# Performance work log

Hardware: AMD Instinct MI355X
Metric: run time of the kernel (lower is better)

Reference implementation:

```python
import jax, jax.numpy as jnp
import numpy as np

B = 16384          # batch (parallel envs)
D_OBS = 512        # num_actor_obs
A = 32             # num_actions
E = 8              # num_experts
K = 2              # top_k
GH = [256, 128]    # gating hidden dims
EH = [1024, 512, 256]  # expert hidden dims


def _linear_init(key, fan_in, fan_out, extra=()):
    kw, kb = jax.random.split(key)
    scale = 1.0 / np.sqrt(fan_in)
    w = jax.random.uniform(kw, extra + (fan_in, fan_out), jnp.float32, -scale, scale)
    b = jax.random.uniform(kb, extra + (fan_out,), jnp.float32, -scale, scale)
    return w, b


def setup_inputs() -> dict:
    key = jax.random.key(0)
    ks = jax.random.split(key, 8)
    obs = jax.random.normal(ks[0], (B, D_OBS), jnp.float32)
    # gating network: D_OBS -> 256 -> 128 -> E
    gw1, gb1 = _linear_init(ks[1], D_OBS, GH[0])
    gw2, gb2 = _linear_init(ks[2], GH[0], GH[1])
    gw3, gb3 = _linear_init(ks[3], GH[1], E)
    # experts (stacked over expert axis): D_OBS -> 1024 -> 512 -> 256 -> A
    ew1, eb1 = _linear_init(ks[4], D_OBS, EH[0], (E,))
    ew2, eb2 = _linear_init(ks[5], EH[0], EH[1], (E,))
    ew3, eb3 = _linear_init(ks[6], EH[1], EH[2], (E,))
    ew4, eb4 = _linear_init(ks[7], EH[2], A, (E,))
    return {
        "observations": obs,
        "gw1": gw1, "gb1": gb1, "gw2": gw2, "gb2": gb2, "gw3": gw3, "gb3": gb3,
        "ew1": ew1, "eb1": eb1, "ew2": ew2, "eb2": eb2,
        "ew3": ew3, "eb3": eb3, "ew4": ew4, "eb4": eb4,
    }


def reference(observations, gw1, gb1, gw2, gb2, gw3, gb3,
              ew1, eb1, ew2, eb2, ew3, eb3, ew4, eb4):
    elu = jax.nn.elu
    # --- gating network ---
    g = elu(observations @ gw1 + gb1)
    g = elu(g @ gw2 + gb2)
    gate_logits = g @ gw3 + gb3                      # [B, E]
    gate_probs = jax.nn.softmax(gate_logits, axis=-1)
    # --- top-k selection and renormalization ---
    topk_w, topk_idx = jax.lax.top_k(gate_probs, K)  # [B, K]
    topk_w = topk_w / jnp.sum(topk_w, axis=-1, keepdims=True)
    # --- run all experts as batched GEMMs (same math as masked dispatch) ---
    h = elu(jnp.einsum('bi,eio->beo', observations, ew1) + eb1)  # [B, E, 1024]
    h = elu(jnp.einsum('beo,eoh->beh', h, ew2) + eb2)            # [B, E, 512]
    h = elu(jnp.einsum('beh,ehf->bef', h, ew3) + eb3)            # [B, E, 256]
    expert_out = jnp.einsum('bef,efa->bea', h, ew4) + eb4        # [B, E, A]
    # --- weighted combine over selected experts ---
    onehot = jax.nn.one_hot(topk_idx, E, dtype=topk_w.dtype)     # [B, K, E]
    combine_w = jnp.einsum('bk,bke->be', topk_w, onehot)         # [B, E]
    action_mean = jnp.einsum('be,bea->ba', combine_w, expert_out)  # [B, A]
    return action_mean
```

## Files before the change

### kernel.cpp

```cpp
#include <hip/hip_runtime.h>
#include <hip/hip_bf16.h>

typedef __bf16 v8bf __attribute__((ext_vector_type(8)));
typedef float  v4f  __attribute__((ext_vector_type(4)));
typedef unsigned int v4u __attribute__((ext_vector_type(4)));

#define B_ROWS 16384
#define NSLOTS 32768
#define MAXTILES 264
#define CSTRIDE 136

#define OFF_W1T   0u
#define OFF_W2T   8388608u
#define OFF_W3T   16777216u
#define OFF_W4T   18874368u
#define OFF_META  19005440u
#define OFF_SEL   19009536u
#define OFF_W01   19075072u
#define OFF_ROWL  19206144u
#define OFF_WL    19337216u
#define OFF_Q     19468288u
#define OFF_G1    OFF_Q
#define OFF_G2    (OFF_Q + 16777216u)
#define OFF_X1    OFF_Q
#define OFF_H2    OFF_Q
#define OFF_EO    OFF_Q
#define OFF_H1    (OFF_Q + 33554432u)
#define OFF_H3    OFF_H1
#define WS_NEED   (OFF_H1 + 67108864u)

#undef  OFF_H2
#undef  OFF_EO
#define OFF_H2B   (OFF_H1 + 67108864u)
#define OFF_EO2   OFF_Q
#undef  WS_NEED
#define WS_NEED   (OFF_H2B + 33554432u)


__device__ __forceinline__ void gload_lds16(const void* g, void* l) {
  __builtin_amdgcn_global_load_lds(
      (const __attribute__((address_space(1))) void*)g,
      (__attribute__((address_space(3))) void*)l, 16, 0, 0);
}

__device__ __forceinline__ float elu_f(float x) {
  return x > 0.f ? x : expm1f(x);
}

__global__ __launch_bounds__(256) void transpose_all(
    const float* __restrict__ ew1, const float* __restrict__ ew2,
    const float* __restrict__ ew3, const float* __restrict__ ew4,
    __hip_bfloat16* __restrict__ W1T, __hip_bfloat16* __restrict__ W2T,
    __hip_bfloat16* __restrict__ W3T, __hip_bfloat16* __restrict__ W4T) {
  __shared__ __align__(16) float tile[32][33];
  int b = blockIdx.x;
  const float* src; __hip_bfloat16* dst; int R, C, gxs, tps, idx;
  if (b < 4096)      { src = ew1; dst = W1T; R = 512;  C = 1024; gxs = 4; tps = 9; idx = b; }
  else if (b < 8192) { src = ew2; dst = W2T; R = 1024; C = 512;  gxs = 5; tps = 9; idx = b - 4096; }
  else if (b < 9216) { src = ew3; dst = W3T; R = 512;  C = 256;  gxs = 4; tps = 7; idx = b - 8192; }
  else               { src = ew4; dst = W4T; R = 256;  C = 32;   gxs = 3; tps = 3; idx = b - 9216; }
  int e = idx >> tps, tt = idx & ((1 << tps) - 1);
  int r0 = (tt & ((1 << gxs) - 1)) * 32, c0 = (tt >> gxs) * 32;
  src += (size_t)e * R * C;
  dst += (size_t)e * R * C;
  int tr = threadIdx.x >> 5, tc = threadIdx.x & 31;
#pragma unroll
  for (int q = 0; q < 4; ++q)
    tile[tr + 8*q][tc] = src[(size_t)(r0 + tr + 8*q) * C + c0 + tc];
  __syncthreads();
#pragma unroll
  for (int q = 0; q < 4; ++q)
    dst[(size_t)(c0 + tr + 8*q) * R + r0 + tc] = __float2bfloat16(tile[tc][tr + 8*q]);
}

__global__ __launch_bounds__(256) void sgemm_elu(
    const float* __restrict__ A, const float* __restrict__ Bm,
    const float* __restrict__ bias, float* __restrict__ C,
    int M, int N, int K) {
  __shared__ __align__(16) float sA[16][132];
  __shared__ __align__(16) float sB[16][68];
  int tid = threadIdx.x;
  int tx = tid & 15, ty = tid >> 4;
  int m0 = blockIdx.x * 128, n0 = blockIdx.y * 64;
  float acc[8][4] = {};
  for (int k0 = 0; k0 < K; k0 += 16) {
    {
      int m = tid >> 1, ks = (tid & 1) * 8;
      const float* ap = &A[(size_t)(m0 + m) * K + k0 + ks];
      float4 v0 = *(const float4*)ap;
      float4 v1 = *(const float4*)(ap + 4);
      sA[ks+0][m] = v0.x; sA[ks+1][m] = v0.y; sA[ks+2][m] = v0.z; sA[ks+3][m] = v0.w;
      sA[ks+4][m] = v1.x; sA[ks+5][m] = v1.y; sA[ks+6][m] = v1.z; sA[ks+7][m] = v1.w;
    }
    {
      int kr = tid >> 4, nn = (tid & 15) * 4;
      *(float4*)&sB[kr][nn] = *(const float4*)&Bm[(size_t)(k0 + kr) * N + n0 + nn];
    }
    __syncthreads();
#pragma unroll
    for (int kk = 0; kk < 16; ++kk) {
      float a[8], b[4];
      *(float4*)&a[0] = *(const float4*)&sA[kk][ty*8];
      *(float4*)&a[4] = *(const float4*)&sA[kk][ty*8+4];
      *(float4*)&b[0] = *(const float4*)&sB[kk][tx*4];
#pragma unroll
      for (int i = 0; i < 8; ++i)
#pragma unroll
        for (int j = 0; j < 4; ++j)
          acc[i][j] = fmaf(a[i], b[j], acc[i][j]);
    }
    __syncthreads();
  }
  float bs[4];
#pragma unroll
  for (int j = 0; j < 4; ++j) bs[j] = bias[n0 + tx*4 + j];
#pragma unroll
  for (int i = 0; i < 8; ++i) {
    int m = m0 + ty*8 + i;
    float4 o;
    o.x = elu_f(acc[i][0] + bs[0]);
    o.y = elu_f(acc[i][1] + bs[1]);
    o.z = elu_f(acc[i][2] + bs[2]);
    o.w = elu_f(acc[i][3] + bs[3]);
    *(float4*)&C[(size_t)m * N + n0 + tx*4] = o;
  }
}

__global__ __launch_bounds__(256) void gate3_topk(
    const float* __restrict__ G2, const float* __restrict__ gw3,
    const float* __restrict__ gb3, int* __restrict__ sel01,
    float2* __restrict__ w01, int* __restrict__ meta) {
  __shared__ __align__(16) float g2t[64][132];
  __shared__ __align__(16) float w3[1024];
  __shared__ float b3[8];
  __shared__ int lc[8];
  int tid = threadIdx.x;
  int row0 = blockIdx.x * 64;
  {
    int r = tid >> 5, f = (tid & 31) * 4;
#pragma unroll
    for (int rr = 0; rr < 64; rr += 8)
      *(float4*)&g2t[r + rr][f] = *(const float4*)&G2[(size_t)(row0 + r + rr) * 128 + f];
  }
  ((float4*)w3)[tid] = ((const float4*)gw3)[tid];
  if (tid < 8) { b3[tid] = gb3[tid]; lc[tid] = 0; }
  __syncthreads();
  if (tid < 64) {
    int row = row0 + tid;
    float lg[8];
#pragma unroll
    for (int e = 0; e < 8; ++e) lg[e] = b3[e];
    for (int k = 0; k < 128; ++k) {
      float x = g2t[tid][k];
#pragma unroll
      for (int e = 0; e < 8; ++e) lg[e] = fmaf(x, w3[k*8 + e], lg[e]);
    }
    float mx = lg[0];
#pragma unroll
    for (int e = 1; e < 8; ++e) mx = fmaxf(mx, lg[e]);
    float p[8], s = 0.f;
#pragma unroll
    for (int e = 0; e < 8; ++e) { p[e] = expf(lg[e] - mx); s += p[e]; }
    float inv = 1.f / s;
#pragma unroll
    for (int e = 0; e < 8; ++e) p[e] *= inv;
    int i0 = 0; float v0 = p[0];
#pragma unroll
    for (int e = 1; e < 8; ++e) if (p[e] > v0) { v0 = p[e]; i0 = e; }
    int i1 = -1; float v1 = -1.f;
#pragma unroll
    for (int e = 0; e < 8; ++e) if (e != i0 && p[e] > v1) { v1 = p[e]; i1 = e; }
    float sw = 1.f / (v0 + v1);
    sel01[row] = i0 | (i1 << 8);
    w01[row] = make_float2(v0 * sw, v1 * sw);
    atomicAdd(&lc[i0], 1);
    atomicAdd(&lc[i1], 1);
  }
  __syncthreads();
  if (tid < 8) atomicAdd(&meta[1 + tid], lc[tid]);
}

__global__ void build_tiles(int* __restrict__ meta) {
  if (threadIdx.x != 0) return;
  int base = 0, nt = 0;
  for (int e = 0; e < 8; ++e) {
    int c = meta[1 + e];
    meta[17 + e] = base;
    for (int j = 0; j < c; j += 128) {
      meta[32 + nt]  = e;
      meta[296 + nt] = base + j;
      meta[560 + nt] = (c - j < 128) ? (c - j) : 128;
      nt++;
    }
    base += c;
  }
  meta[0] = nt;
}

__global__ __launch_bounds__(256) void scatter_rows(
    const int* __restrict__ sel01, float2* __restrict__ w01,
    int* __restrict__ meta, int* __restrict__ rowlist, float* __restrict__ wlist) {
  __shared__ int lc[8];
  __shared__ int gb[8];
  int tid = threadIdx.x;
  if (tid < 8) lc[tid] = 0;
  __syncthreads();
  int row = blockIdx.x * 256 + tid;
  int s = sel01[row];
  int e0 = s & 255, e1 = (s >> 8) & 255;
  float2 w = w01[row];
  int l0 = atomicAdd(&lc[e0], 1);
  int l1 = atomicAdd(&lc[e1], 1);
  __syncthreads();
  if (tid < 8) gb[tid] = atomicAdd(&meta[9 + tid], lc[tid]);
  __syncthreads();
  int s0 = meta[17 + e0] + gb[e0] + l0;
  int s1 = meta[17 + e1] + gb[e1] + l1;
  rowlist[s0] = row; wlist[s0] = w.x;
  rowlist[s1] = row; wlist[s1] = w.y;
  ((int2*)w01)[row] = make_int2(s0, s1);
}

__global__ __launch_bounds__(256) void gather_convert(
    const float* __restrict__ obs, const int* __restrict__ rowlist,
    __hip_bfloat16* __restrict__ X1) {
  int tid = threadIdx.x;
  int slot = blockIdx.x * 4 + (tid >> 6);
  int l = tid & 63;
  int row = rowlist[slot];
  const float* src = obs + (size_t)row * 512 + l * 8;
  float4 a = *(const float4*)src;
  float4 b = *(const float4*)(src + 4);
  union { __hip_bfloat16 h[8]; v4u u; } t;
  t.h[0] = __float2bfloat16(a.x); t.h[1] = __float2bfloat16(a.y);
  t.h[2] = __float2bfloat16(a.z); t.h[3] = __float2bfloat16(a.w);
  t.h[4] = __float2bfloat16(b.x); t.h[5] = __float2bfloat16(b.y);
  t.h[6] = __float2bfloat16(b.z); t.h[7] = __float2bfloat16(b.w);
  *(v4u*)(X1 + (size_t)slot * 512 + l * 8) = t.u;
}

__global__ __launch_bounds__(256) void moe_gemm(
    const __hip_bfloat16* __restrict__ A, const __hip_bfloat16* __restrict__ BT,
    const float* __restrict__ bias, __hip_bfloat16* __restrict__ C,
    const int* __restrict__ meta, int N, int K, int lgNB) {
  int b = blockIdx.x;
  int c = b & 7;
  int j = (b >> 3) & ((1 << lgNB) - 1);
  int m = b >> (3 + lgNB);
  int t = m * 8 + c;
  if (t >= meta[0]) return;
  int e    = meta[32 + t];
  int m0   = meta[296 + t];
  int rows = meta[560 + t];
  int n0   = j * 128;

  __shared__ __align__(16) char smem[CSTRIDE * 64 * 2 > 16384 ? CSTRIDE * 64 * 2 : 16384];
  __hip_bfloat16* sA  = (__hip_bfloat16*)smem;
  __hip_bfloat16* sB  = (__hip_bfloat16*)(smem + 8192);
  __hip_bfloat16* cst = (__hip_bfloat16*)smem;

  int tid = threadIdx.x;
  int w = tid >> 6, l = tid & 63;
  int lr = l >> 2;
  int lk = (l & 3) * 8;
  int wm = w >> 1, wn = w & 1;
  int ml = l & 15, kq = l >> 4;

  const __hip_bfloat16* BTe = BT + (size_t)e * N * K;
  v4f acc[4][4] = {};

  for (int k0 = 0; k0 < K; k0 += 32) {
#pragma unroll
    for (int it = 0; it < 2; ++it) {
      int r = it * 64 + w * 16 + lr;
      int gr = m0 + (r < rows ? r : rows - 1);
      gload_lds16(A + (size_t)gr * K + k0 + lk, &sA[(it * 64 + w * 16) * 32]);
    }
#pragma unroll
    for (int it = 0; it < 2; ++it) {
      int r = it * 64 + w * 16 + lr;
      gload_lds16(BTe + (size_t)(n0 + r) * K + k0 + lk, &sB[(it * 64 + w * 16) * 32]);
    }
    __syncthreads();
    v8bf af[4], bf[4];
#pragma unroll
    for (int i = 0; i < 4; ++i)
      af[i] = *(const v8bf*)&sA[(wm * 64 + i * 16 + ml) * 32 + kq * 8];
#pragma unroll
    for (int jj = 0; jj < 4; ++jj)
      bf[jj] = *(const v8bf*)&sB[(wn * 64 + jj * 16 + ml) * 32 + kq * 8];
#pragma unroll
    for (int i = 0; i < 4; ++i)
#pragma unroll
      for (int jj = 0; jj < 4; ++jj)
        acc[i][jj] = __builtin_amdgcn_mfma_f32_16x16x32_bf16(af[i], bf[jj], acc[i][jj], 0, 0, 0);
    __syncthreads();
  }

  float bs[4];
#pragma unroll
  for (int jj = 0; jj < 4; ++jj)
    bs[jj] = bias[(size_t)e * N + n0 + wn * 64 + jj * 16 + ml];

#pragma unroll
  for (int h = 0; h < 2; ++h) {
    if (wm == h) {
#pragma unroll
      for (int i = 0; i < 4; ++i)
#pragma unroll
        for (int jj = 0; jj < 4; ++jj)
#pragma unroll
          for (int r = 0; r < 4; ++r)
            cst[(i * 16 + kq * 4 + r) * CSTRIDE + wn * 64 + jj * 16 + ml] =
                __float2bfloat16(elu_f(acc[i][jj][r] + bs[jj]));
    }
    __syncthreads();
#pragma unroll
    for (int q = 0; q < 4; ++q) {
      int z = q * 256 + tid;
      int row = z >> 4, ch = z & 15;
      int rl = h * 64 + row;
      if (rl < rows) {
        v4u v = *(const v4u*)&cst[row * CSTRIDE + ch * 8];
        __builtin_nontemporal_store(
            v, (v4u*)&C[(size_t)(m0 + rl) * N + n0 + ch * 8]);
      }
    }
    __syncthreads();
  }
}

__global__ __launch_bounds__(256) void l4_gemm(
    const __hip_bfloat16* __restrict__ H3, const __hip_bfloat16* __restrict__ W4T,
    const float* __restrict__ eb4, const int* __restrict__ meta,
    float* __restrict__ EO) {
  int t = blockIdx.x;
  if (t >= meta[0]) return;
  int e = meta[32 + t], m0 = meta[296 + t], rows = meta[560 + t];
  __shared__ __align__(16) __hip_bfloat16 sW[32 * 264];
  int tid = threadIdx.x;
  {
    const uint4* src = (const uint4*)(W4T + (size_t)e * 8192);
#pragma unroll
    for (int q = 0; q < 4; ++q) {
      int c = tid + 256 * q;
      int r = c >> 5, col = (c & 31) * 8;
      *(uint4*)&sW[r * 264 + col] = src[c];
    }
  }
  __syncthreads();
  int w = tid >> 6, l = tid & 63;
  int ml = l & 15, kq = l >> 4;
  v4f acc[2][2] = {};
  const __hip_bfloat16* Abase = H3 + (size_t)m0 * 256;
#pragma unroll
  for (int k0 = 0; k0 < 256; k0 += 32) {
    v8bf af[2], bf[2];
#pragma unroll
    for (int i = 0; i < 2; ++i) {
      int r = w * 32 + i * 16 + ml;
      int rr = r < rows ? r : 0;
      af[i] = *(const v8bf*)(Abase + (size_t)rr * 256 + k0 + kq * 8);
    }
#pragma unroll
    for (int j = 0; j < 2; ++j)
      bf[j] = *(const v8bf*)&sW[(j * 16 + ml) * 264 + k0 + kq * 8];
#pragma unroll
    for (int i = 0; i < 2; ++i)
#pragma unroll
      for (int j = 0; j < 2; ++j)
        acc[i][j] = __builtin_amdgcn_mfma_f32_16x16x32_bf16(af[i], bf[j], acc[i][j], 0, 0, 0);
  }
#pragma unroll
  for (int j = 0; j < 2; ++j) {
    int col = j * 16 + ml;
    float bs = eb4[e * 32 + col];
#pragma unroll
    for (int i = 0; i < 2; ++i) {
#pragma unroll
      for (int r = 0; r < 4; ++r) {
        int rl = w * 32 + i * 16 + kq * 4 + r;
        if (rl < rows)
          EO[(size_t)(m0 + rl) * 32 + col] = acc[i][j][r] + bs;
      }
    }
  }
}

__global__ __launch_bounds__(256) void combine_out(
    const float* __restrict__ EO, const int2* __restrict__ invmap,
    const float* __restrict__ wlist, float* __restrict__ out) {
  int gid = blockIdx.x * 256 + threadIdx.x;
  int row = gid >> 3, q = (gid & 7) * 4;
  int2 s = invmap[row];
  float w0 = wlist[s.x], w1 = wlist[s.y];
  float4 a = *(const float4*)(EO + (size_t)s.x * 32 + q);
  float4 b = *(const float4*)(EO + (size_t)s.y * 32 + q);
  float4 o;
  o.x = w0 * a.x + w1 * b.x;
  o.y = w0 * a.y + w1 * b.y;
  o.z = w0 * a.z + w1 * b.z;
  o.w = w0 * a.w + w1 * b.w;
  *(float4*)(out + (size_t)row * 32 + q) = o;
}

extern "C" void kernel_launch(void* const* d_in, const int* in_sizes, int n_in,
                              void* d_out, int out_size, void* d_ws, size_t ws_size,
                              hipStream_t stream) {
  const float* obs = (const float*)d_in[0];
  const float* gw1 = (const float*)d_in[1];
  const float* gb1 = (const float*)d_in[2];
  const float* gw2 = (const float*)d_in[3];
  const float* gb2 = (const float*)d_in[4];
  const float* gw3 = (const float*)d_in[5];
  const float* gb3 = (const float*)d_in[6];
  const float* ew1 = (const float*)d_in[7];
  const float* eb1 = (const float*)d_in[8];
  const float* ew2 = (const float*)d_in[9];
  const float* eb2 = (const float*)d_in[10];
  const float* ew3 = (const float*)d_in[11];
  const float* eb3 = (const float*)d_in[12];
  const float* ew4 = (const float*)d_in[13];
  const float* eb4 = (const float*)d_in[14];

  if (ws_size < (size_t)WS_NEED) return;

  char* ws = (char*)d_ws;
  __hip_bfloat16* W1T = (__hip_bfloat16*)(ws + OFF_W1T);
  __hip_bfloat16* W2T = (__hip_bfloat16*)(ws + OFF_W2T);
  __hip_bfloat16* W3T = (__hip_bfloat16*)(ws + OFF_W3T);
  __hip_bfloat16* W4T = (__hip_bfloat16*)(ws + OFF_W4T);
  int*    meta    = (int*)(ws + OFF_META);
  int*    sel01   = (int*)(ws + OFF_SEL);
  float2* w01     = (float2*)(ws + OFF_W01);
  int*    rowlist = (int*)(ws + OFF_ROWL);
  float*  wlist   = (float*)(ws + OFF_WL);
  float*  G1      = (float*)(ws + OFF_G1);
  float*  G2      = (float*)(ws + OFF_G2);
  __hip_bfloat16* X1 = (__hip_bfloat16*)(ws + OFF_X1);
  __hip_bfloat16* H1 = (__hip_bfloat16*)(ws + OFF_H1);
  __hip_bfloat16* H2 = (__hip_bfloat16*)(ws + OFF_H2B);
  __hip_bfloat16* H3 = (__hip_bfloat16*)(ws + OFF_H3);
  float* EO       = (float*)(ws + OFF_EO2);
  float* outp = (float*)d_out;

  (void)hipMemsetAsync(meta, 0, 128, stream);

  transpose_all<<<9280, 256, 0, stream>>>(ew1, ew2, ew3, ew4, W1T, W2T, W3T, W4T);

  sgemm_elu<<<dim3(128, 4), 256, 0, stream>>>(obs, gw1, gb1, G1, B_ROWS, 256, 512);
  sgemm_elu<<<dim3(128, 2), 256, 0, stream>>>(G1, gw2, gb2, G2, B_ROWS, 128, 256);
  gate3_topk<<<256, 256, 0, stream>>>(G2, gw3, gb3, sel01, w01, meta);
  build_tiles<<<1, 64, 0, stream>>>(meta);
  scatter_rows<<<64, 256, 0, stream>>>(sel01, w01, meta, rowlist, wlist);
  gather_convert<<<8192, 256, 0, stream>>>(obs, rowlist, X1);

  moe_gemm<<<MAXTILES * 8, 256, 0, stream>>>(X1, W1T, eb1, H1, meta, 1024, 512, 3);
  moe_gemm<<<MAXTILES * 4, 256, 0, stream>>>(H1, W2T, eb2, H2, meta, 512, 1024, 2);
  moe_gemm<<<MAXTILES * 2, 256, 0, stream>>>(H2, W3T, eb3, H3, meta, 256, 512, 1);
  l4_gemm<<<MAXTILES, 256, 0, stream>>>(H3, W4T, eb4, meta, EO);
  combine_out<<<512, 256, 0, stream>>>(EO, (const int2*)w01, wlist, outp);
}
```

Measured before the change: 481.4 us.

## Double-buffer LDS tiles in MoE GEMM with XOR-swizzled K chunks

Restructures the MoE expert GEMM main loop to use two LDS buffers, issuing global-to-LDS loads for the next K tile before computing on the current one, which cuts one barrier per iteration. The K-chunk placement is XOR-swizzled by row on both the load and read sides to reduce LDS bank conflicts. Global row pointers are hoisted out of the loop. LDS use doubles to 32KB, which may lower occupancy.

After: 460.4 us. 4.3% less time.

```diff
diff --git a/kernel.cpp b/kernel.cpp
--- a/kernel.cpp
+++ b/kernel.cpp
@@ -23,17 +23,10 @@
 #define OFF_G1    OFF_Q
 #define OFF_G2    (OFF_Q + 16777216u)
 #define OFF_X1    OFF_Q
-#define OFF_H2    OFF_Q
-#define OFF_EO    OFF_Q
+#define OFF_EO2   OFF_Q
 #define OFF_H1    (OFF_Q + 33554432u)
 #define OFF_H3    OFF_H1
-#define WS_NEED   (OFF_H1 + 67108864u)
-
-#undef  OFF_H2
-#undef  OFF_EO
 #define OFF_H2B   (OFF_H1 + 67108864u)
-#define OFF_EO2   OFF_Q
-#undef  WS_NEED
 #define WS_NEED   (OFF_H2B + 33554432u)
 
 
@@ -254,48 +247,65 @@
   int rows = meta[560 + t];
   int n0   = j * 128;
 
-  __shared__ __align__(16) char smem[CSTRIDE * 64 * 2 > 16384 ? CSTRIDE * 64 * 2 : 16384];
-  __hip_bfloat16* sA  = (__hip_bfloat16*)smem;
-  __hip_bfloat16* sB  = (__hip_bfloat16*)(smem + 8192);
+  __shared__ __align__(16) char smem[32768];
   __hip_bfloat16* cst = (__hip_bfloat16*)smem;
 
   int tid = threadIdx.x;
   int w = tid >> 6, l = tid & 63;
   int lr = l >> 2;
-  int lk = (l & 3) * 8;
+  int csw = ((l & 3) ^ ((l >> 3) & 3)) * 8;
   int wm = w >> 1, wn = w & 1;
   int ml = l & 15, kq = l >> 4;
+  int key = (ml >> 1) & 3;
 
   const __hip_bfloat16* BTe = BT + (size_t)e * N * K;
+  int ra0 = w * 16 + lr, ra1 = 64 + w * 16 + lr;
+  const __hip_bfloat16* gA0 = A + (size_t)(m0 + (ra0 < rows ? ra0 : rows - 1)) * K + csw;
+  const __hip_bfloat16* gA1 = A + (size_t)(m0 + (ra1 < rows ? ra1 : rows - 1)) * K + csw;
+  const __hip_bfloat16* gB0 = BTe + (size_t)(n0 + ra0) * K + csw;
+  const __hip_bfloat16* gB1 = BTe + (size_t)(n0 + ra1) * K + csw;
+
   v4f acc[4][4] = {};
-
-  for (int k0 = 0; k0 < K; k0 += 32) {
-#pragma unroll
-    for (int it = 0; it < 2; ++it) {
-      int r = it * 64 + w * 16 + lr;
-      int gr = m0 + (r < rows ? r : rows - 1);
-      gload_lds16(A + (size_t)gr * K + k0 + lk, &sA[(it * 64 + w * 16) * 32]);
-    }
-#pragma unroll
-    for (int it = 0; it < 2; ++it) {
-      int r = it * 64 + w * 16 + lr;
-      gload_lds16(BTe + (size_t)(n0 + r) * K + k0 + lk, &sB[(it * 64 + w * 16) * 32]);
-    }
+  int nIter = K >> 5;
+
+  {
+    __hip_bfloat16* sA = (__hip_bfloat16*)smem;
+    __hip_bfloat16* sB = (__hip_bfloat16*)(smem + 8192);
+    gload_lds16(gA0, &sA[(w * 16) * 32]);
+    gload_lds16(gA1, &sA[(64 + w * 16) * 32]);
+    gload_lds16(gB0, &sB[(w * 16) * 32]);
+    gload_lds16(gB1, &sB[(64 + w * 16) * 32]);
+  }
+
+  for (int it = 0; it < nIter; ++it) {
     __syncthreads();
+    int cur = (it & 1) * 16384;
+    if (it + 1 < nIter) {
+      int nxt = ((it + 1) & 1) * 16384;
+      int k0 = (it + 1) << 5;
+      __hip_bfloat16* sA = (__hip_bfloat16*)(smem + nxt);
+      __hip_bfloat16* sB = (__hip_bfloat16*)(smem + nxt + 8192);
+      gload_lds16(gA0 + k0, &sA[(w * 16) * 32]);
+      gload_lds16(gA1 + k0, &sA[(64 + w * 16) * 32]);
+      gload_lds16(gB0 + k0, &sB[(w * 16) * 32]);
+      gload_lds16(gB1 + k0, &sB[(64 + w * 16) * 32]);
+    }
+    const __hip_bfloat16* sA = (const __hip_bfloat16*)(smem + cur);
+    const __hip_bfloat16* sB = (const __hip_bfloat16*)(smem + cur + 8192);
     v8bf af[4], bf[4];
 #pragma unroll
     for (int i = 0; i < 4; ++i)
-      af[i] = *(const v8bf*)&sA[(wm * 64 + i * 16 + ml) * 32 + kq * 8];
+      af[i] = *(const v8bf*)&sA[(wm * 64 + i * 16 + ml) * 32 + ((kq ^ key)) * 8];
 #pragma unroll
     for (int jj = 0; jj < 4; ++jj)
-      bf[jj] = *(const v8bf*)&sB[(wn * 64 + jj * 16 + ml) * 32 + kq * 8];
+      bf[jj] = *(const v8bf*)&sB[(wn * 64 + jj * 16 + ml) * 32 + ((kq ^ key)) * 8];
 #pragma unroll
     for (int i = 0; i < 4; ++i)
 #pragma unroll
       for (int jj = 0; jj < 4; ++jj)
         acc[i][jj] = __builtin_amdgcn_mfma_f32_16x16x32_bf16(af[i], bf[jj], acc[i][jj], 0, 0, 0);
-    __syncthreads();
-  }
+  }
+  __syncthreads();
 
   float bs[4];
 #pragma unroll
```
